# Kernel optimization log

Hardware: AMD Instinct MI355X
Metric: run time of the kernel (lower is better)

The kernel has to match this reference:

```python
import jax, jax.numpy as jnp
import numpy as np

EPS = 1e-12  # keras K.l2_normalize epsilon


def setup_inputs() -> dict:
    key = jax.random.key(0)
    k1, k2, k3 = jax.random.split(key, 3)
    B, T, C = 4, 4096, 64
    L = 15
    N_NODE = 64
    x = jax.random.normal(k1, (B, T, C), dtype=jnp.float32)
    w = jax.random.normal(k2, (L,), dtype=jnp.float32)            # st_conv_filter_one
    conv_w = jax.random.normal(k3, (C * C, N_NODE), dtype=jnp.float32) * 0.02  # 1x1 conv kernel
    conv_b = jnp.zeros((N_NODE,), dtype=jnp.float32)
    return {"x": x, "w": w, "conv_w": conv_w, "conv_b": conv_b}


def reference(x, w, conv_w, conv_b):
    B, T, C = x.shape
    L = w.shape[0]
    pad = L // 2
    # ZeroPadding1D(local_size//2): pad time axis on both sides
    x_pad = jnp.pad(x, ((0, 0), (pad, pad), (0, 0)))  # [B, T+2*pad, C]
    # Gather sliding windows: [B, T, L, C]
    idx = jnp.arange(T)[:, None] + jnp.arange(L)[None, :]
    xw = x_pad[:, idx, :]
    # Bilinear form per frame: X^T diag(w) X -> [B, T, C, C]
    bil = jnp.einsum('btlc,l,btld->btcd', xw, w, xw)
    # Flatten to [B, T, C*C]
    feat = bil.reshape(B, T, C * C)
    # L2 normalize along last axis (keras K.l2_normalize)
    sq = jnp.sum(feat * feat, axis=-1, keepdims=True)
    feat = feat * jax.lax.rsqrt(jnp.maximum(sq, EPS))
    # 1x1 Conv1D(n_node) == per-frame dense layer
    out = jnp.einsum('btk,kn->btn', feat, conv_w) + conv_b
    return out
```

## Files before the change

### kernel.cpp

```cpp
#include <hip/hip_runtime.h>
#include <stdint.h>

#define T_DIM 4096
#define S_DIM 16384
#define EPSF 1e-12f

typedef __attribute__((ext_vector_type(8))) short   short8v;
typedef __attribute__((ext_vector_type(4))) float   float4v;
typedef __attribute__((ext_vector_type(4))) uint32_t uint4v;

__device__ __forceinline__ unsigned short f2bf_rne(float f) {
    uint32_t u = __builtin_bit_cast(uint32_t, f);
    return (unsigned short)((u + 0x7fffu + ((u >> 16) & 1u)) >> 16);
}
__device__ __forceinline__ uint32_t cvtpk(float lo, float hi) {
    uint32_t r;
    asm("v_cvt_pk_bf16_f32 %0, %1, %2" : "=v"(r) : "v"(lo), "v"(hi));
    return r;
}

#define GLOAD_LDS16(gsrc, ldst)                                                     \
    __builtin_amdgcn_global_load_lds(                                               \
        (const __attribute__((address_space(1))) void*)(gsrc),                      \
        (__attribute__((address_space(3))) void*)(ldst), 16, 0, 0)

__global__ __launch_bounds__(256) void k_convert(const float* __restrict__ conv_w,
                                                 unsigned short* __restrict__ wfrag) {
    __shared__ unsigned short lb[64][65];
    int tid = threadIdx.x;
    int cc  = blockIdx.x;
    for (int i = tid; i < 4096; i += 256) {
        lb[i >> 6][i & 63] = f2bf_rne(conv_w[((size_t)cc << 12) + i]);
    }
    __syncthreads();
    for (int gi = tid; gi < 512; gi += 256) {
        int nt = gi >> 7, h = (gi >> 6) & 1, ln = gi & 63;
        int n  = (nt << 4) + (ln & 15);
        int kb = (h << 5) + ((ln >> 4) << 3);
        uint4v u;
        #pragma unroll
        for (int q = 0; q < 4; ++q)
            u[q] = (uint32_t)lb[kb + 2 * q][n] | ((uint32_t)lb[kb + 2 * q + 1][n] << 16);
        *(uint4v*)(wfrag + ((size_t)cc << 12) + (gi << 3)) = u;
    }
}

__global__ __launch_bounds__(256) void k_dotsP(const float* __restrict__ x,
                                               const float* __restrict__ w,
                                               float* __restrict__ P) {
    __shared__ float xt[78 * 65];
    __shared__ float pd[4][64][17];
    __shared__ float dsq[64][17];
    int tid = threadIdx.x, lane = tid & 63, wv = tid >> 6;
    int s0 = blockIdx.x << 6;
    int bt0 = s0 & (T_DIM - 1);
    for (int i = tid; i < 78 * 16; i += 256) {
        int r = i >> 4, c4 = (i & 15) << 2;
        float4v v = {0.f, 0.f, 0.f, 0.f};
        if (bt0 + r < T_DIM) v = *(const float4v*)(x + (((size_t)(s0 + r)) << 6) + c4);
        #pragma unroll
        for (int q = 0; q < 4; ++q) xt[r * 65 + c4 + q] = v[q];
    }
    __syncthreads();
    float acc[15];
    #pragma unroll
    for (int j = 0; j < 15; ++j) acc[j] = 0.f;
    int c0 = wv << 4;
    for (int c = c0; c < c0 + 16; ++c) {
        const float* base = &xt[lane * 65 + c];
        float xl = base[0];
        #pragma unroll
        for (int j = 0; j < 15; ++j) acc[j] += xl * base[j * 65];
    }
    #pragma unroll
    for (int j = 0; j < 15; ++j) pd[wv][lane][j] = acc[j];
    __syncthreads();
    for (int i = tid; i < 960; i += 256) {
        int s = i & 63, j = i >> 6;
        float d = pd[0][s][j] + pd[1][s][j] + pd[2][s][j] + pd[3][s][j];
        dsq[s][j] = d * d;
    }
    __syncthreads();
    for (int i = tid; i < 960; i += 256) {
        int s = i & 63, l = i >> 6;
        float sum = w[l] * dsq[s][0];
        for (int j = 1; j <= 14 - l; ++j) sum += 2.f * w[l + j] * dsq[s][j];
        P[(size_t)l * S_DIM + s0 + s] = sum;
    }
}

__global__ __launch_bounds__(256) void k_rsq(const float* __restrict__ P,
                                             const float* __restrict__ w,
                                             float* __restrict__ rsq) {
    int s = blockIdx.x * 256 + threadIdx.x;
    int t = s & (T_DIM - 1);
    float sum = 0.f;
    #pragma unroll
    for (int l = 0; l < 15; ++l) {
        int tp = t + l - 7;
        if (0 <= tp && tp < T_DIM) sum += w[l] * P[(size_t)l * S_DIM + s + l - 7];
    }
    rsq[s] = rsqrtf(fmaxf(sum, EPSF));
}

__global__ __launch_bounds__(256) void k_gemm(const float* __restrict__ x,
                                              const unsigned short* __restrict__ wfrag,
                                              float* __restrict__ g) {
    __shared__ alignas(16) unsigned short wbuf[2][4096];
    int tid = threadIdx.x, lane = tid & 63, wv = tid >> 6;
    int split = blockIdx.x & 3;
    int m0 = (blockIdx.x >> 2) << 7;
    int c0 = split << 4;

    int arow = lane & 15;
    int kgrp = (lane >> 4) << 3;
    const float* xr0 = x + (((size_t)(m0 + (wv << 5) + arow)) << 6);
    const float* xr1 = x + (((size_t)(m0 + (wv << 5) + 16 + arow)) << 6);
    float4v p00a = *(const float4v*)(xr0 + kgrp);
    float4v p01a = *(const float4v*)(xr0 + kgrp + 4);
    float4v p10a = *(const float4v*)(xr0 + 32 + kgrp);
    float4v p11a = *(const float4v*)(xr0 + 36 + kgrp);
    float4v p00b = *(const float4v*)(xr1 + kgrp);
    float4v p01b = *(const float4v*)(xr1 + kgrp + 4);
    float4v p10b = *(const float4v*)(xr1 + 32 + kgrp);
    float4v p11b = *(const float4v*)(xr1 + 36 + kgrp);

    const char* wsb = (const char*)wfrag;
#define STAGE_CHUNK(bi, c) do {                                                   \
        GLOAD_LDS16(wsb + ((size_t)(c) << 13) + (tid << 4),                       \
                    (char*)&wbuf[bi][0] + (wv << 10));                            \
        GLOAD_LDS16(wsb + ((size_t)(c) << 13) + 4096 + (tid << 4),                \
                    (char*)&wbuf[bi][0] + 4096 + (wv << 10));                     \
    } while (0)

    float4v accA[4], accB[4];
    #pragma unroll
    for (int nt = 0; nt < 4; ++nt)
        #pragma unroll
        for (int j = 0; j < 4; ++j) { accA[nt][j] = 0.f; accB[nt][j] = 0.f; }

    const short8v* fb0 = (const short8v*)&wbuf[0][0];
    const short8v* fb1 = (const short8v*)&wbuf[1][0];

    STAGE_CHUNK(0, c0);
    __syncthreads();

    #pragma unroll 2
    for (int ci = 0; ci < 16; ++ci) {
        if (ci < 15) STAGE_CHUNK((ci + 1) & 1, c0 + ci + 1);

        const short8v* fb = (ci & 1) ? fb1 : fb0;
        short8v b0 = fb[lane];
        short8v b1 = fb[64 + lane];
        short8v b2 = fb[128 + lane];
        short8v b3 = fb[192 + lane];
        short8v b4 = fb[256 + lane];
        short8v b5 = fb[320 + lane];
        short8v b6 = fb[384 + lane];
        short8v b7 = fb[448 + lane];

        {
            float xc = xr0[c0 + ci];
            union { uint32_t u[4]; short8v s; } a0, a1;
            float4v q0 = p00a * xc, q1 = p01a * xc, q2 = p10a * xc, q3 = p11a * xc;
            a0.u[0] = cvtpk(q0[0], q0[1]); a0.u[1] = cvtpk(q0[2], q0[3]);
            a0.u[2] = cvtpk(q1[0], q1[1]); a0.u[3] = cvtpk(q1[2], q1[3]);
            a1.u[0] = cvtpk(q2[0], q2[1]); a1.u[1] = cvtpk(q2[2], q2[3]);
            a1.u[2] = cvtpk(q3[0], q3[1]); a1.u[3] = cvtpk(q3[2], q3[3]);
            accA[0] = __builtin_amdgcn_mfma_f32_16x16x32_bf16(a0.s, b0, accA[0], 0, 0, 0);
            accA[0] = __builtin_amdgcn_mfma_f32_16x16x32_bf16(a1.s, b1, accA[0], 0, 0, 0);
            accA[1] = __builtin_amdgcn_mfma_f32_16x16x32_bf16(a0.s, b2, accA[1], 0, 0, 0);
            accA[1] = __builtin_amdgcn_mfma_f32_16x16x32_bf16(a1.s, b3, accA[1], 0, 0, 0);
            accA[2] = __builtin_amdgcn_mfma_f32_16x16x32_bf16(a0.s, b4, accA[2], 0, 0, 0);
            accA[2] = __builtin_amdgcn_mfma_f32_16x16x32_bf16(a1.s, b5, accA[2], 0, 0, 0);
            accA[3] = __builtin_amdgcn_mfma_f32_16x16x32_bf16(a0.s, b6, accA[3], 0, 0, 0);
            accA[3] = __builtin_amdgcn_mfma_f32_16x16x32_bf16(a1.s, b7, accA[3], 0, 0, 0);
        }
        {
            float xc = xr1[c0 + ci];
            union { uint32_t u[4]; short8v s; } a0, a1;
            float4v q0 = p00b * xc, q1 = p01b * xc, q2 = p10b * xc, q3 = p11b * xc;
            a0.u[0] = cvtpk(q0[0], q0[1]); a0.u[1] = cvtpk(q0[2], q0[3]);
            a0.u[2] = cvtpk(q1[0], q1[1]); a0.u[3] = cvtpk(q1[2], q1[3]);
            a1.u[0] = cvtpk(q2[0], q2[1]); a1.u[1] = cvtpk(q2[2], q2[3]);
            a1.u[2] = cvtpk(q3[0], q3[1]); a1.u[3] = cvtpk(q3[2], q3[3]);
            accB[0] = __builtin_amdgcn_mfma_f32_16x16x32_bf16(a0.s, b0, accB[0], 0, 0, 0);
            accB[0] = __builtin_amdgcn_mfma_f32_16x16x32_bf16(a1.s, b1, accB[0], 0, 0, 0);
            accB[1] = __builtin_amdgcn_mfma_f32_16x16x32_bf16(a0.s, b2, accB[1], 0, 0, 0);
            accB[1] = __builtin_amdgcn_mfma_f32_16x16x32_bf16(a1.s, b3, accB[1], 0, 0, 0);
            accB[2] = __builtin_amdgcn_mfma_f32_16x16x32_bf16(a0.s, b4, accB[2], 0, 0, 0);
            accB[2] = __builtin_amdgcn_mfma_f32_16x16x32_bf16(a1.s, b5, accB[2], 0, 0, 0);
            accB[3] = __builtin_amdgcn_mfma_f32_16x16x32_bf16(a0.s, b6, accB[3], 0, 0, 0);
            accB[3] = __builtin_amdgcn_mfma_f32_16x16x32_bf16(a1.s, b7, accB[3], 0, 0, 0);
        }

        __syncthreads();
    }
#undef STAGE_CHUNK

    float* gp = g + (size_t)split * ((size_t)S_DIM * 64);
    int col0 = lane & 15;
    int crowA = m0 + (wv << 5) + ((lane >> 4) << 2);
    int crowB = crowA + 16;
    #pragma unroll
    for (int nt = 0; nt < 4; ++nt)
        #pragma unroll
        for (int j = 0; j < 4; ++j) {
            gp[((size_t)(crowA + j) << 6) + (nt << 4) + col0] = accA[nt][j];
            gp[((size_t)(crowB + j) << 6) + (nt << 4) + col0] = accB[nt][j];
        }
}

__global__ __launch_bounds__(256) void k_final(const float* __restrict__ g,
                                               const float* __restrict__ rsq,
                                               const float* __restrict__ w,
                                               const float* __restrict__ conv_b,
                                               float* __restrict__ out) {
    int lane = threadIdx.x & 63, wv = threadIdx.x >> 6;
    int wid = blockIdx.x * 4 + wv;
    int t0 = wid << 4;
    int bt0 = t0 & (T_DIM - 1);
    const size_t SP = (size_t)S_DIM * 64;
    float r[30];
    #pragma unroll
    for (int i = 0; i < 30; ++i) {
        int tr = bt0 - 7 + i;
        r[i] = 0.f;
        if (0 <= tr && tr < T_DIM) {
            const float* p = g + (((size_t)(t0 - 7 + i)) << 6) + lane;
            r[i] = (p[0] + p[SP]) + (p[2 * SP] + p[3 * SP]);
        }
    }
    float bn = conv_b[lane];
    #pragma unroll
    for (int i = 0; i < 16; ++i) {
        float acc = 0.f;
        #pragma unroll
        for (int l = 0; l < 15; ++l) acc += w[l] * r[i + l];
        out[(((size_t)(t0 + i)) << 6) + lane] = acc * rsq[t0 + i] + bn;
    }
}

extern "C" void kernel_launch(void* const* d_in, const int* in_sizes, int n_in,
                              void* d_out, int out_size, void* d_ws, size_t ws_size,
                              hipStream_t stream) {
    const float* x      = (const float*)d_in[0];
    const float* w      = (const float*)d_in[1];
    const float* conv_w = (const float*)d_in[2];
    const float* conv_b = (const float*)d_in[3];
    float* out = (float*)d_out;

    char* ws = (char*)d_ws;
    unsigned short* wfrag = (unsigned short*)ws;
    float* g              = (float*)(ws + 524288);
    float* P              = (float*)(ws + 524288 + 16777216);
    float* rsq            = P + (size_t)15 * S_DIM;

    hipLaunchKernelGGL(k_convert, dim3(64),  dim3(256), 0, stream, conv_w, wfrag);
    hipLaunchKernelGGL(k_dotsP,   dim3(256), dim3(256), 0, stream, x, w, P);
    hipLaunchKernelGGL(k_gemm,    dim3(512), dim3(256), 0, stream, x, wfrag, g);
    hipLaunchKernelGGL(k_rsq,     dim3(64),  dim3(256), 0, stream, P, w, rsq);
    hipLaunchKernelGGL(k_final,   dim3(256), dim3(256), 0, stream, g, rsq, w, conv_b, out);
}
```

Before: 54.82 us.

## Halve GEMM row tile and split output columns across waves for more blocks

The GEMM block now covers 64 rows instead of 128. Its four waves are split two by two over row groups and output-column halves, so each wave holds 4 accumulators instead of 8. The grid doubles to 1024 blocks and launch bounds request 4 blocks per CU. The aim is higher occupancy and better latency hiding in exchange for less reuse of each staged weight chunk. Total weight staging traffic per row doubles, and each wave now recomputes the bf16 A fragments for only half the MFMA work.

```diff
diff --git a/kernel.cpp b/kernel.cpp
--- a/kernel.cpp
+++ b/kernel.cpp
@@ -103,19 +103,22 @@
     rsq[s] = rsqrtf(fmaxf(sum, EPSF));
 }
 
-__global__ __launch_bounds__(256) void k_gemm(const float* __restrict__ x,
-                                              const unsigned short* __restrict__ wfrag,
-                                              float* __restrict__ g) {
+__global__ __launch_bounds__(256, 4) void k_gemm(const float* __restrict__ x,
+                                                 const unsigned short* __restrict__ wfrag,
+                                                 float* __restrict__ g) {
     __shared__ alignas(16) unsigned short wbuf[2][4096];
     int tid = threadIdx.x, lane = tid & 63, wv = tid >> 6;
     int split = blockIdx.x & 3;
-    int m0 = (blockIdx.x >> 2) << 7;
+    int m0 = (blockIdx.x >> 2) << 6;
     int c0 = split << 4;
 
-    int arow = lane & 15;
-    int kgrp = (lane >> 4) << 3;
-    const float* xr0 = x + (((size_t)(m0 + (wv << 5) + arow)) << 6);
-    const float* xr1 = x + (((size_t)(m0 + (wv << 5) + 16 + arow)) << 6);
+    int arow   = lane & 15;
+    int kgrp   = (lane >> 4) << 3;
+    int rgbase = (wv & 1) << 5;
+    int ntb    = (wv >> 1) << 1;
+
+    const float* xr0 = x + (((size_t)(m0 + rgbase + arow)) << 6);
+    const float* xr1 = x + (((size_t)(m0 + rgbase + 16 + arow)) << 6);
     float4v p00a = *(const float4v*)(xr0 + kgrp);
     float4v p01a = *(const float4v*)(xr0 + kgrp + 4);
     float4v p10a = *(const float4v*)(xr0 + 32 + kgrp);
@@ -133,11 +136,13 @@
                     (char*)&wbuf[bi][0] + 4096 + (wv << 10));                     \
     } while (0)
 
-    float4v accA[4], accB[4];
-    #pragma unroll
-    for (int nt = 0; nt < 4; ++nt)
-        #pragma unroll
-        for (int j = 0; j < 4; ++j) { accA[nt][j] = 0.f; accB[nt][j] = 0.f; }
+    float4v acc[2][2];
+    #pragma unroll
+    for (int rg = 0; rg < 2; ++rg)
+        #pragma unroll
+        for (int q = 0; q < 2; ++q)
+            #pragma unroll
+            for (int j = 0; j < 4; ++j) acc[rg][q][j] = 0.f;
 
     const short8v* fb0 = (const short8v*)&wbuf[0][0];
     const short8v* fb1 = (const short8v*)&wbuf[1][0];
@@ -150,14 +155,10 @@
         if (ci < 15) STAGE_CHUNK((ci + 1) & 1, c0 + ci + 1);
 
         const short8v* fb = (ci & 1) ? fb1 : fb0;
-        short8v b0 = fb[lane];
-        short8v b1 = fb[64 + lane];
-        short8v b2 = fb[128 + lane];
-        short8v b3 = fb[192 + lane];
-        short8v b4 = fb[256 + lane];
-        short8v b5 = fb[320 + lane];
-        short8v b6 = fb[384 + lane];
-        short8v b7 = fb[448 + lane];
+        short8v b00 = fb[(ntb << 7) + lane];
+        short8v b01 = fb[(ntb << 7) + 64 + lane];
+        short8v b10 = fb[((ntb + 1) << 7) + lane];
+        short8v b11 = fb[((ntb + 1) << 7) + 64 + lane];
 
         {
             float xc = xr0[c0 + ci];
@@ -167,14 +168,10 @@
             a0.u[2] = cvtpk(q1[0], q1[1]); a0.u[3] = cvtpk(q1[2], q1[3]);
             a1.u[0] = cvtpk(q2[0], q2[1]); a1.u[1] = cvtpk(q2[2], q2[3]);
             a1.u[2] = cvtpk(q3[0], q3[1]); a1.u[3] = cvtpk(q3[2], q3[3]);
-            accA[0] = __builtin_amdgcn_mfma_f32_16x16x32_bf16(a0.s, b0, accA[0], 0, 0, 0);
-            accA[0] = __builtin_amdgcn_mfma_f32_16x16x32_bf16(a1.s, b1, accA[0], 0, 0, 0);
-            accA[1] = __builtin_amdgcn_mfma_f32_16x16x32_bf16(a0.s, b2, accA[1], 0, 0, 0);
-            accA[1] = __builtin_amdgcn_mfma_f32_16x16x32_bf16(a1.s, b3, accA[1], 0, 0, 0);
-            accA[2] = __builtin_amdgcn_mfma_f32_16x16x32_bf16(a0.s, b4, accA[2], 0, 0, 0);
-            accA[2] = __builtin_amdgcn_mfma_f32_16x16x32_bf16(a1.s, b5, accA[2], 0, 0, 0);
-            accA[3] = __builtin_amdgcn_mfma_f32_16x16x32_bf16(a0.s, b6, accA[3], 0, 0, 0);
-            accA[3] = __builtin_amdgcn_mfma_f32_16x16x32_bf16(a1.s, b7, accA[3], 0, 0, 0);
+            acc[0][0] = __builtin_amdgcn_mfma_f32_16x16x32_bf16(a0.s, b00, acc[0][0], 0, 0, 0);
+            acc[0][0] = __builtin_amdgcn_mfma_f32_16x16x32_bf16(a1.s, b01, acc[0][0], 0, 0, 0);
+            acc[0][1] = __builtin_amdgcn_mfma_f32_16x16x32_bf16(a0.s, b10, acc[0][1], 0, 0, 0);
+            acc[0][1] = __builtin_amdgcn_mfma_f32_16x16x32_bf16(a1.s, b11, acc[0][1], 0, 0, 0);
         }
         {
             float xc = xr1[c0 + ci];
@@ -184,14 +181,10 @@
             a0.u[2] = cvtpk(q1[0], q1[1]); a0.u[3] = cvtpk(q1[2], q1[3]);
             a1.u[0] = cvtpk(q2[0], q2[1]); a1.u[1] = cvtpk(q2[2], q2[3]);
             a1.u[2] = cvtpk(q3[0], q3[1]); a1.u[3] = cvtpk(q3[2], q3[3]);
-            accB[0] = __builtin_amdgcn_mfma_f32_16x16x32_bf16(a0.s, b0, accB[0], 0, 0, 0);
-            accB[0] = __builtin_amdgcn_mfma_f32_16x16x32_bf16(a1.s, b1, accB[0], 0, 0, 0);
-            accB[1] = __builtin_amdgcn_mfma_f32_16x16x32_bf16(a0.s, b2, accB[1], 0, 0, 0);
-            accB[1] = __builtin_amdgcn_mfma_f32_16x16x32_bf16(a1.s, b3, accB[1], 0, 0, 0);
-            accB[2] = __builtin_amdgcn_mfma_f32_16x16x32_bf16(a0.s, b4, accB[2], 0, 0, 0);
-            accB[2] = __builtin_amdgcn_mfma_f32_16x16x32_bf16(a1.s, b5, accB[2], 0, 0, 0);
-            accB[3] = __builtin_amdgcn_mfma_f32_16x16x32_bf16(a0.s, b6, accB[3], 0, 0, 0);
-            accB[3] = __builtin_amdgcn_mfma_f32_16x16x32_bf16(a1.s, b7, accB[3], 0, 0, 0);
+            acc[1][0] = __builtin_amdgcn_mfma_f32_16x16x32_bf16(a0.s, b00, acc[1][0], 0, 0, 0);
+            acc[1][0] = __builtin_amdgcn_mfma_f32_16x16x32_bf16(a1.s, b01, acc[1][0], 0, 0, 0);
+            acc[1][1] = __builtin_amdgcn_mfma_f32_16x16x32_bf16(a0.s, b10, acc[1][1], 0, 0, 0);
+            acc[1][1] = __builtin_amdgcn_mfma_f32_16x16x32_bf16(a1.s, b11, acc[1][1], 0, 0, 0);
         }
 
         __syncthreads();
@@ -200,15 +193,17 @@
 
     float* gp = g + (size_t)split * ((size_t)S_DIM * 64);
     int col0 = lane & 15;
-    int crowA = m0 + (wv << 5) + ((lane >> 4) << 2);
-    int crowB = crowA + 16;
-    #pragma unroll
-    for (int nt = 0; nt < 4; ++nt)
-        #pragma unroll
-        for (int j = 0; j < 4; ++j) {
-            gp[((size_t)(crowA + j) << 6) + (nt << 4) + col0] = accA[nt][j];
-            gp[((size_t)(crowB + j) << 6) + (nt << 4) + col0] = accB[nt][j];
-        }
+    #pragma unroll
+    for (int rg = 0; rg < 2; ++rg) {
+        int crow = m0 + rgbase + (rg << 4) + ((lane >> 4) << 2);
+        #pragma unroll
+        for (int q = 0; q < 2; ++q) {
+            int ncol = ((ntb + q) << 4) + col0;
+            #pragma unroll
+            for (int j = 0; j < 4; ++j)
+                gp[((size_t)(crow + j) << 6) + ncol] = acc[rg][q][j];
+        }
+    }
 }
 
 __global__ __launch_bounds__(256) void k_final(const float* __restrict__ g,
@@ -256,9 +251,9 @@
     float* P              = (float*)(ws + 524288 + 16777216);
     float* rsq            = P + (size_t)15 * S_DIM;
 
-    hipLaunchKernelGGL(k_convert, dim3(64),  dim3(256), 0, stream, conv_w, wfrag);
-    hipLaunchKernelGGL(k_dotsP,   dim3(256), dim3(256), 0, stream, x, w, P);
-    hipLaunchKernelGGL(k_gemm,    dim3(512), dim3(256), 0, stream, x, wfrag, g);
-    hipLaunchKernelGGL(k_rsq,     dim3(64),  dim3(256), 0, stream, P, w, rsq);
-    hipLaunchKernelGGL(k_final,   dim3(256), dim3(256), 0, stream, g, rsq, w, conv_b, out);
-}
+    hipLaunchKernelGGL(k_convert, dim3(64),   dim3(256), 0, stream, conv_w, wfrag);
+    hipLaunchKernelGGL(k_dotsP,   dim3(256),  dim3(256), 0, stream, x, w, P);
+    hipLaunchKernelGGL(k_gemm,    dim3(1024), dim3(256), 0, stream, x, wfrag, g);
+    hipLaunchKernelGGL(k_rsq,     dim3(64),   dim3(256), 0, stream, P, w, rsq);
+    hipLaunchKernelGGL(k_final,   dim3(256),  dim3(256), 0, stream, g, rsq, w, conv_b, out);
+}
```

Result: slower. 60.43 us (+10.2%).
